# Kernel optimization log

Hardware: AMD Instinct MI355X
Metric: run time of the kernel (lower is better)

## Reference

```python
import jax, jax.numpy as jnp
import numpy as np

B, N, V, H = 8, 2048, 256, 1024
EPS = 1e-5
NEG = -1e9


def _layernorm(x, g, b):
    m = jnp.mean(x, axis=-1, keepdims=True)
    v = jnp.mean((x - m) ** 2, axis=-1, keepdims=True)
    return (x - m) / jnp.sqrt(v + EPS) * g + b


def setup_inputs() -> dict:
    key = jax.random.key(0)
    ks = jax.random.split(key, 10)
    tril = jnp.tril(jnp.ones((N, N), jnp.float32))
    return {
        "h": jax.random.normal(ks[0], (B, N, V), jnp.float32),
        "mask_one": tril,                      # keep causal entries
        "mask_zero": NEG * (1.0 - tril),       # -inf-ish above diagonal
        "ln_attn_g": jnp.ones((V,), jnp.float32),
        "ln_attn_b": jnp.zeros((V,), jnp.float32),
        "ln_mlp_g": jnp.ones((V,), jnp.float32),
        "ln_mlp_b": jnp.zeros((V,), jnp.float32),
        "wv": jax.random.normal(ks[1], (V,), jnp.float32),
        "wv_bos": jax.random.normal(ks[2], (V,), jnp.float32),
        "wo_w": jax.random.normal(ks[3], (V, V), jnp.float32) / np.sqrt(V),
        "qk_bos": jax.random.normal(ks[4], (V,), jnp.float32),
        "qk_previous": jax.random.normal(ks[5], (V,), jnp.float32),
        "qk_direction": jnp.ones((V,), jnp.float32),  # middel_layer=False, frozen
        "w1": jax.random.normal(ks[6], (H, V), jnp.float32) / np.sqrt(V),
        "w2": jax.random.normal(ks[7], (V, H), jnp.float32) / np.sqrt(H),
    }


def reference(h, mask_one, mask_zero, ln_attn_g, ln_attn_b, ln_mlp_g, ln_mlp_b,
              wv, wv_bos, wo_w, qk_bos, qk_previous, qk_direction, w1, w2):
    b, n, v = h.shape
    # mask blends LayerNorm only into row 0 (BOS position)
    attn_input = h.at[:, 0, :].set(_layernorm(h[:, 0, :], ln_attn_g, ln_attn_b))
    # value states: diag(wv) on positions 1.., wo(wv_bos) at position 0
    values = attn_input[:, 1:, :] * wv                      # [B, N-1, V]
    v_bos = wo_w @ wv_bos                                   # Linear(bias=False)
    values = jnp.concatenate(
        [jnp.broadcast_to(v_bos, (b, 1, v)), values], axis=1)  # [B, N, V]
    # sparse QK logits: column 0 term + sub-diagonal term, densified then masked
    col0 = (attn_input @ qk_bos) * (attn_input[:, 0, :] @ qk_direction)[:, None]  # [B, N]
    d = attn_input @ qk_previous                            # [B, N]
    qk = jnp.zeros((b, n, n), h.dtype).at[:, :, 0].add(col0)
    idx = jnp.arange(1, n)
    qk = qk.at[:, idx, idx - 1].add(d[:, 1:])               # row r, col r-1 = d[:, r]
    qk = qk * mask_one + mask_zero
    attn_out = jax.nn.softmax(qk, axis=-1) @ values         # [B, N, V]
    # FFN branch with its own BOS-only LayerNorm blend
    mlp_input = h.at[:, 0, :].set(_layernorm(h[:, 0, :], ln_mlp_g, ln_mlp_b))
    mlp_out = jax.nn.relu(mlp_input @ w1.T) @ w2.T          # [B, N, V]
    return attn_out + mlp_out
```

## Files before the change

kernel.cpp:

```cpp
#include <hip/hip_runtime.h>
#include <hip/hip_bf16.h>

#define BB 8
#define NN 2048
#define VV 256
#define HH 1024
#define CHK 64
#define RPC 32
constexpr float EPS = 1e-5f;

typedef __attribute__((ext_vector_type(4))) float floatx4;
typedef __attribute__((ext_vector_type(8))) short short8;

__device__ __forceinline__ void load_lds16(const void* g, void* l) {
    __builtin_amdgcn_global_load_lds((const __attribute__((address_space(1))) void*)g,
                                     (__attribute__((address_space(3))) void*)l, 16, 0, 0);
}

__global__ void prep_kernel(const float* __restrict__ h,
                            const float* __restrict__ g_attn, const float* __restrict__ b_attn,
                            const float* __restrict__ g_mlp,  const float* __restrict__ b_mlp,
                            const float* __restrict__ qk_dir,
                            const float* __restrict__ wo_w,  const float* __restrict__ wv_bos,
                            float* __restrict__ attn_row0, float* __restrict__ mlp_row0,
                            float* __restrict__ v_bos, float* __restrict__ sum0)
{
    int t = threadIdx.x;
    __shared__ float red[VV];
    if (blockIdx.x < BB) {
        int b = blockIdx.x;
        float x = h[(size_t)b * NN * VV + t];
        red[t] = x; __syncthreads();
        for (int s = 128; s > 0; s >>= 1) { if (t < s) red[t] += red[t + s]; __syncthreads(); }
        float m = red[0] * (1.0f / VV); __syncthreads();
        float xc = x - m;
        red[t] = xc * xc; __syncthreads();
        for (int s = 128; s > 0; s >>= 1) { if (t < s) red[t] += red[t + s]; __syncthreads(); }
        float var = red[0] * (1.0f / VV); __syncthreads();
        float inv = 1.0f / sqrtf(var + EPS);
        float an = xc * inv * g_attn[t] + b_attn[t];
        float mn = xc * inv * g_mlp[t] + b_mlp[t];
        attn_row0[b * VV + t] = an;
        mlp_row0[b * VV + t]  = mn;
        red[t] = an * qk_dir[t]; __syncthreads();
        for (int s = 128; s > 0; s >>= 1) { if (t < s) red[t] += red[t + s]; __syncthreads(); }
        if (t == 0) sum0[b] = red[0];
    } else {
        const float4* wp = reinterpret_cast<const float4*>(wo_w + (size_t)t * VV);
        const float4* vp = reinterpret_cast<const float4*>(wv_bos);
        float acc = 0.f;
        for (int j = 0; j < VV / 4; ++j) {
            float4 a = wp[j], b = vp[j];
            acc += a.x * b.x + a.y * b.y + a.z * b.z + a.w * b.w;
        }
        v_bos[t] = acc;
    }
}

__global__ void qkw_kernel(const float* __restrict__ h,
                           const float* __restrict__ qk_bos, const float* __restrict__ qk_prev,
                           const float* __restrict__ sum0,
                           float* __restrict__ w0, float* __restrict__ wprev, float* __restrict__ wz)
{
    int wave = threadIdx.x >> 6, lane = threadIdx.x & 63;
    int gid = blockIdx.x * 4 + wave;
    int b = gid >> 11, r = gid & (NN - 1);
    const float4* hp = reinterpret_cast<const float4*>(h + (size_t)gid * VV);
    float4 x = hp[lane];
    float4 qb = reinterpret_cast<const float4*>(qk_bos)[lane];
    float4 qp = reinterpret_cast<const float4*>(qk_prev)[lane];
    float s1 = x.x * qb.x + x.y * qb.y + x.z * qb.z + x.w * qb.w;
    float s2 = x.x * qp.x + x.y * qp.y + x.z * qp.z + x.w * qp.w;
    for (int off = 32; off > 0; off >>= 1) {
        s1 += __shfl_down(s1, off);
        s2 += __shfl_down(s2, off);
    }
    if (lane == 0) {
        float W0, WP, WZ;
        if (r == 0) { W0 = 1.f; WP = 0.f; WZ = 0.f; }
        else if (r == 1) {
            float a = s1 * sum0[b] + s2;
            float m = fmaxf(a, 0.f);
            float ea = expf(a - m), ez = expf(-m);
            float Z = ea + ez;
            W0 = ea / Z; WZ = ez / Z; WP = WZ;
        } else {
            float a = s1 * sum0[b];
            float dd = s2;
            float m = fmaxf(fmaxf(a, dd), 0.f);
            float ea = expf(a - m), ed = expf(dd - m), ez = expf(-m);
            float Z = ea + ed + (float)(r - 1) * ez;
            W0 = ea / Z; WP = ed / Z; WZ = ez / Z;
        }
        w0[gid] = W0; wprev[gid] = WP; wz[gid] = WZ;
    }
}

__global__ void chunksum_kernel(const float* __restrict__ h, const float* __restrict__ wv,
                                float* __restrict__ chunkSum)
{
    int b = blockIdx.x / CHK, c = blockIdx.x % CHK;
    int v = threadIdx.x;
    float wvv = wv[v];
    float s = 0.f;
    int r0 = c * RPC;
    for (int r = r0; r < r0 + RPC; ++r)
        if (r >= 1) s += h[((size_t)b * NN + r) * VV + v] * wvv;
    chunkSum[(b * CHK + c) * VV + v] = s;
}

__global__ void chunkscan_kernel(float* __restrict__ chunkSum)
{
    int b = blockIdx.x, v = threadIdx.x;
    float run = 0.f;
    for (int c = 0; c < CHK; ++c) {
        int idx = (b * CHK + c) * VV + v;
        float t = chunkSum[idx];
        chunkSum[idx] = run;
        run += t;
    }
}

__global__ void attn_kernel(const float* __restrict__ h, const float* __restrict__ wv,
                            const float* __restrict__ v_bos,
                            const float* __restrict__ w0, const float* __restrict__ wprev,
                            const float* __restrict__ wz, const float* __restrict__ chunkSum,
                            float* __restrict__ out)
{
    int b = blockIdx.x / CHK, c = blockIdx.x % CHK;
    int v = threadIdx.x;
    float wvv = wv[v], vb = v_bos[v];
    float S = chunkSum[(b * CHK + c) * VV + v];
    int r0 = c * RPC;
    float prev = (r0 == 0) ? 0.f : h[((size_t)b * NN + r0 - 1) * VV + v] * wvv;
    for (int r = r0; r < r0 + RPC; ++r) {
        size_t idx = ((size_t)b * NN + r) * VV + v;
        float o;
        if (r == 0) {
            o = vb;
            prev = 0.f;
        } else {
            float val = h[idx] * wvv;
            S += val;
            int wi = b * NN + r;
            o = w0[wi] * vb + (wprev[wi] - wz[wi]) * prev + wz[wi] * S;
            prev = val;
        }
        out[idx] = o;
    }
}

__global__ void cvt_x_kernel(const float* __restrict__ h, const float* __restrict__ mlp_row0,
                             __hip_bfloat16* __restrict__ Xb)
{
    int i = blockIdx.x * blockDim.x + threadIdx.x;
    int e = i * 4;
    int v = e & (VV - 1);
    int row = e >> 8;
    int r = row & (NN - 1), b = row >> 11;
    const float* src = (r == 0) ? (mlp_row0 + b * VV + v) : (h + (size_t)row * VV + v);
    float4 x = *reinterpret_cast<const float4*>(src);
    Xb[e + 0] = __float2bfloat16(x.x);
    Xb[e + 1] = __float2bfloat16(x.y);
    Xb[e + 2] = __float2bfloat16(x.z);
    Xb[e + 3] = __float2bfloat16(x.w);
}

__global__ void cvt_w_kernel(const float* __restrict__ w1, const float* __restrict__ w2,
                             __hip_bfloat16* __restrict__ w1b, __hip_bfloat16* __restrict__ w2b)
{
    int i = (blockIdx.x * blockDim.x + threadIdx.x) * 4;
    const float* src;
    __hip_bfloat16* dst;
    if (i < HH * VV) { src = w1 + i; dst = w1b + i; }
    else             { src = w2 + (i - HH * VV); dst = w2b + (i - HH * VV); }
    float4 x = *reinterpret_cast<const float4*>(src);
    dst[0] = __float2bfloat16(x.x);
    dst[1] = __float2bfloat16(x.y);
    dst[2] = __float2bfloat16(x.z);
    dst[3] = __float2bfloat16(x.w);
}

template<int BM, int BN, int K, int OUTN, bool FUSE_RELU_BF16>
__global__ __launch_bounds__(256) void mfma_gemm(const short* __restrict__ Ag,
                                                 const short* __restrict__ Bg,
                                                 __hip_bfloat16* __restrict__ Obf,
                                                 float* __restrict__ Ofp)
{
    constexpr int TM = BM / 2, TN = BN / 2;
    constexpr int MI = TM / 16, NJ = TN / 16;
    __shared__ __align__(16) short sA[BM * 32];
    __shared__ __align__(16) short sB[BN * 32];
    int wave = threadIdx.x >> 6, lane = threadIdx.x & 63;
    int wm = wave >> 1, wn = wave & 1;
    int m0 = blockIdx.x * BM, n0 = blockIdx.y * BN;

    int lrow = lane >> 2;
    int lp   = lane & 3;
    int ra   = lane & 15;
    int q    = lane >> 4;

    floatx4 acc[MI][NJ];
#pragma unroll
    for (int i = 0; i < MI; ++i)
#pragma unroll
        for (int j = 0; j < NJ; ++j) acc[i][j] = floatx4{0, 0, 0, 0};

    for (int k0 = 0; k0 < K; k0 += 32) {
#pragma unroll
        for (int i = 0; i < BM / 64; ++i) {
            int g = i * 4 + wave;
            int row = g * 16 + lrow;
            int s = lp ^ ((row >> 1) & 3);
            load_lds16(Ag + (size_t)(m0 + row) * K + k0 + s * 8, sA + g * 512);
        }
#pragma unroll
        for (int i = 0; i < BN / 64; ++i) {
            int g = i * 4 + wave;
            int row = g * 16 + lrow;
            int s = lp ^ ((row >> 1) & 3);
            load_lds16(Bg + (size_t)(n0 + row) * K + k0 + s * 8, sB + g * 512);
        }
        __syncthreads();

        short8 af[MI], bfr[NJ];
#pragma unroll
        for (int i = 0; i < MI; ++i) {
            int m = wm * TM + i * 16 + ra;
            int slot = q ^ ((m >> 1) & 3);
            af[i] = *reinterpret_cast<const short8*>(sA + m * 32 + slot * 8);
        }
#pragma unroll
        for (int j = 0; j < NJ; ++j) {
            int n = wn * TN + j * 16 + ra;
            int slot = q ^ ((n >> 1) & 3);
            bfr[j] = *reinterpret_cast<const short8*>(sB + n * 32 + slot * 8);
        }
#pragma unroll
        for (int i = 0; i < MI; ++i)
#pragma unroll
            for (int j = 0; j < NJ; ++j)
                acc[i][j] = __builtin_amdgcn_mfma_f32_16x16x32_bf16(af[i], bfr[j], acc[i][j], 0, 0, 0);
        __syncthreads();
    }

    int rq = q * 4;
#pragma unroll
    for (int i = 0; i < MI; ++i) {
        int rbase = m0 + wm * TM + i * 16 + rq;
#pragma unroll
        for (int j = 0; j < NJ; ++j) {
            int col = n0 + wn * TN + j * 16 + ra;
#pragma unroll
            for (int reg = 0; reg < 4; ++reg) {
                size_t idx = (size_t)(rbase + reg) * OUTN + col;
                if (FUSE_RELU_BF16)
                    Obf[idx] = __float2bfloat16(fmaxf(acc[i][j][reg], 0.f));
                else
                    Ofp[idx] += acc[i][j][reg];
            }
        }
    }
}

extern "C" void kernel_launch(void* const* d_in, const int* in_sizes, int n_in,
                              void* d_out, int out_size, void* d_ws, size_t ws_size,
                              hipStream_t stream)
{
    const float* h        = (const float*)d_in[0];
    const float* ln_attn_g = (const float*)d_in[3];
    const float* ln_attn_b = (const float*)d_in[4];
    const float* ln_mlp_g  = (const float*)d_in[5];
    const float* ln_mlp_b  = (const float*)d_in[6];
    const float* wv        = (const float*)d_in[7];
    const float* wv_bos    = (const float*)d_in[8];
    const float* wo_w      = (const float*)d_in[9];
    const float* qk_bos    = (const float*)d_in[10];
    const float* qk_prev   = (const float*)d_in[11];
    const float* qk_dir    = (const float*)d_in[12];
    const float* w1        = (const float*)d_in[13];
    const float* w2        = (const float*)d_in[14];
    float* out = (float*)d_out;

    float* attn_row0 = (float*)d_ws;
    float* mlp_row0  = attn_row0 + BB * VV;
    float* v_bos     = mlp_row0 + BB * VV;
    float* sum0      = v_bos + VV;
    float* w0        = sum0 + 8;
    float* wprev     = w0 + BB * NN;
    float* wzz       = wprev + BB * NN;
    float* chunkSum  = wzz + BB * NN;
    __hip_bfloat16* Xb  = (__hip_bfloat16*)(chunkSum + BB * CHK * VV);
    __hip_bfloat16* w1b = Xb + (size_t)BB * NN * VV;
    __hip_bfloat16* w2b = w1b + HH * VV;
    __hip_bfloat16* Yb  = w2b + VV * HH;

    prep_kernel<<<BB + 1, 256, 0, stream>>>(h, ln_attn_g, ln_attn_b, ln_mlp_g, ln_mlp_b,
                                            qk_dir, wo_w, wv_bos,
                                            attn_row0, mlp_row0, v_bos, sum0);
    cvt_x_kernel<<<(BB * NN * VV / 4) / 256, 256, 0, stream>>>(h, mlp_row0, Xb);
    cvt_w_kernel<<<(2 * HH * VV / 4) / 256, 256, 0, stream>>>(w1, w2, w1b, w2b);
    qkw_kernel<<<BB * NN / 4, 256, 0, stream>>>(h, qk_bos, qk_prev, sum0, w0, wprev, wzz);
    chunksum_kernel<<<BB * CHK, 256, 0, stream>>>(h, wv, chunkSum);
    chunkscan_kernel<<<BB, 256, 0, stream>>>(chunkSum);
    attn_kernel<<<BB * CHK, 256, 0, stream>>>(h, wv, v_bos, w0, wprev, wzz, chunkSum, out);

    mfma_gemm<128, 128, VV, HH, true>
        <<<dim3(BB * NN / 128, HH / 128), 256, 0, stream>>>(
            (const short*)Xb, (const short*)w1b, Yb, nullptr);
    mfma_gemm<128, 64, HH, VV, false>
        <<<dim3(BB * NN / 128, VV / 64), 256, 0, stream>>>(
            (const short*)Yb, (const short*)w2b, nullptr, out);
}
```

Measured before the change: 187.7 us.

## Fuse MLP GEMMs into one kernel and merge activation conversion with qk/scan prep

```diff
diff --git a/kernel.cpp b/kernel.cpp
--- a/kernel.cpp
+++ b/kernel.cpp
@@ -57,56 +57,73 @@
     }
 }
 
-__global__ void qkw_kernel(const float* __restrict__ h,
-                           const float* __restrict__ qk_bos, const float* __restrict__ qk_prev,
-                           const float* __restrict__ sum0,
-                           float* __restrict__ w0, float* __restrict__ wprev, float* __restrict__ wz)
-{
+__global__ __launch_bounds__(256) void scan_qkw_cvt_kernel(
+    const float* __restrict__ h, const float* __restrict__ mlp_row0,
+    const float* __restrict__ wv,
+    const float* __restrict__ qk_bos, const float* __restrict__ qk_prev,
+    const float* __restrict__ sum0,
+    short* __restrict__ Xb,
+    float* __restrict__ w0, float* __restrict__ wprev, float* __restrict__ wz,
+    float* __restrict__ chunkSum)
+{
+    __shared__ float lds[4][VV];
     int wave = threadIdx.x >> 6, lane = threadIdx.x & 63;
-    int gid = blockIdx.x * 4 + wave;
-    int b = gid >> 11, r = gid & (NN - 1);
-    const float4* hp = reinterpret_cast<const float4*>(h + (size_t)gid * VV);
-    float4 x = hp[lane];
-    float4 qb = reinterpret_cast<const float4*>(qk_bos)[lane];
-    float4 qp = reinterpret_cast<const float4*>(qk_prev)[lane];
-    float s1 = x.x * qb.x + x.y * qb.y + x.z * qb.z + x.w * qb.w;
-    float s2 = x.x * qp.x + x.y * qp.y + x.z * qp.z + x.w * qp.w;
-    for (int off = 32; off > 0; off >>= 1) {
-        s1 += __shfl_down(s1, off);
-        s2 += __shfl_down(s2, off);
-    }
-    if (lane == 0) {
-        float W0, WP, WZ;
-        if (r == 0) { W0 = 1.f; WP = 0.f; WZ = 0.f; }
-        else if (r == 1) {
-            float a = s1 * sum0[b] + s2;
-            float m = fmaxf(a, 0.f);
-            float ea = expf(a - m), ez = expf(-m);
-            float Z = ea + ez;
-            W0 = ea / Z; WZ = ez / Z; WP = WZ;
-        } else {
-            float a = s1 * sum0[b];
-            float dd = s2;
-            float m = fmaxf(fmaxf(a, dd), 0.f);
-            float ea = expf(a - m), ed = expf(dd - m), ez = expf(-m);
-            float Z = ea + ed + (float)(r - 1) * ez;
-            W0 = ea / Z; WP = ed / Z; WZ = ez / Z;
-        }
-        w0[gid] = W0; wprev[gid] = WP; wz[gid] = WZ;
-    }
-}
-
-__global__ void chunksum_kernel(const float* __restrict__ h, const float* __restrict__ wv,
-                                float* __restrict__ chunkSum)
-{
     int b = blockIdx.x / CHK, c = blockIdx.x % CHK;
+    int r0 = c * RPC + wave * 8;
+    float4 wv4 = reinterpret_cast<const float4*>(wv)[lane];
+    float4 qb4 = reinterpret_cast<const float4*>(qk_bos)[lane];
+    float4 qp4 = reinterpret_cast<const float4*>(qk_prev)[lane];
+    float s0b = sum0[b];
+    float4 vsum = {0.f, 0.f, 0.f, 0.f};
+#pragma unroll
+    for (int rr = 0; rr < 8; ++rr) {
+        int r = r0 + rr;
+        size_t base = ((size_t)b * NN + r) * VV;
+        float4 x = *reinterpret_cast<const float4*>(h + base + lane * 4);
+        float4 xs = x;
+        if (r == 0) xs = *reinterpret_cast<const float4*>(mlp_row0 + b * VV + lane * 4);
+        __hip_bfloat16 c0 = __float2bfloat16(xs.x), c1 = __float2bfloat16(xs.y),
+                       c2 = __float2bfloat16(xs.z), c3 = __float2bfloat16(xs.w);
+        short4 pk;
+        pk.x = *reinterpret_cast<short*>(&c0);
+        pk.y = *reinterpret_cast<short*>(&c1);
+        pk.z = *reinterpret_cast<short*>(&c2);
+        pk.w = *reinterpret_cast<short*>(&c3);
+        *reinterpret_cast<short4*>(Xb + base + lane * 4) = pk;
+        if (r != 0) {
+            vsum.x += x.x * wv4.x; vsum.y += x.y * wv4.y;
+            vsum.z += x.z * wv4.z; vsum.w += x.w * wv4.w;
+        }
+        float s1 = x.x * qb4.x + x.y * qb4.y + x.z * qb4.z + x.w * qb4.w;
+        float s2 = x.x * qp4.x + x.y * qp4.y + x.z * qp4.z + x.w * qp4.w;
+        for (int off = 32; off > 0; off >>= 1) {
+            s1 += __shfl_down(s1, off);
+            s2 += __shfl_down(s2, off);
+        }
+        if (lane == 0) {
+            int gid = b * NN + r;
+            float W0, WP, WZ;
+            if (r == 0) { W0 = 1.f; WP = 0.f; WZ = 0.f; }
+            else if (r == 1) {
+                float a = s1 * s0b + s2;
+                float m = fmaxf(a, 0.f);
+                float ea = expf(a - m), ez = expf(-m);
+                float Z = ea + ez;
+                W0 = ea / Z; WZ = ez / Z; WP = WZ;
+            } else {
+                float a = s1 * s0b;
+                float m = fmaxf(fmaxf(a, s2), 0.f);
+                float ea = expf(a - m), ed = expf(s2 - m), ez = expf(-m);
+                float Z = ea + ed + (float)(r - 1) * ez;
+                W0 = ea / Z; WP = ed / Z; WZ = ez / Z;
+            }
+            w0[gid] = W0; wprev[gid] = WP; wz[gid] = WZ;
+        }
+    }
+    reinterpret_cast<float4*>(lds[wave])[lane] = vsum;
+    __syncthreads();
     int v = threadIdx.x;
-    float wvv = wv[v];
-    float s = 0.f;
-    int r0 = c * RPC;
-    for (int r = r0; r < r0 + RPC; ++r)
-        if (r >= 1) s += h[((size_t)b * NN + r) * VV + v] * wvv;
-    chunkSum[(b * CHK + c) * VV + v] = s;
+    chunkSum[((size_t)b * CHK + c) * VV + v] = lds[0][v] + lds[1][v] + lds[2][v] + lds[3][v];
 }
 
 __global__ void chunkscan_kernel(float* __restrict__ chunkSum)
@@ -150,22 +167,6 @@
     }
 }
 
-__global__ void cvt_x_kernel(const float* __restrict__ h, const float* __restrict__ mlp_row0,
-                             __hip_bfloat16* __restrict__ Xb)
-{
-    int i = blockIdx.x * blockDim.x + threadIdx.x;
-    int e = i * 4;
-    int v = e & (VV - 1);
-    int row = e >> 8;
-    int r = row & (NN - 1), b = row >> 11;
-    const float* src = (r == 0) ? (mlp_row0 + b * VV + v) : (h + (size_t)row * VV + v);
-    float4 x = *reinterpret_cast<const float4*>(src);
-    Xb[e + 0] = __float2bfloat16(x.x);
-    Xb[e + 1] = __float2bfloat16(x.y);
-    Xb[e + 2] = __float2bfloat16(x.z);
-    Xb[e + 3] = __float2bfloat16(x.w);
-}
-
 __global__ void cvt_w_kernel(const float* __restrict__ w1, const float* __restrict__ w2,
                              __hip_bfloat16* __restrict__ w1b, __hip_bfloat16* __restrict__ w2b)
 {
@@ -181,83 +182,118 @@
     dst[3] = __float2bfloat16(x.w);
 }
 
-template<int BM, int BN, int K, int OUTN, bool FUSE_RELU_BF16>
-__global__ __launch_bounds__(256) void mfma_gemm(const short* __restrict__ Ag,
-                                                 const short* __restrict__ Bg,
-                                                 __hip_bfloat16* __restrict__ Obf,
-                                                 float* __restrict__ Ofp)
-{
-    constexpr int TM = BM / 2, TN = BN / 2;
-    constexpr int MI = TM / 16, NJ = TN / 16;
-    __shared__ __align__(16) short sA[BM * 32];
-    __shared__ __align__(16) short sB[BN * 32];
+__global__ __launch_bounds__(512) void mlp_fused(const short* __restrict__ Xb,
+                                                 const short* __restrict__ w1b,
+                                                 const short* __restrict__ w2b,
+                                                 float* __restrict__ out)
+{
+    __shared__ __align__(16) short sX[64 * 256];
+    __shared__ __align__(16) short sW1[64 * 256];
+    __shared__ __align__(16) short sW2[256 * 64];
+    __shared__ __align__(16) short sY[64 * 64];
     int wave = threadIdx.x >> 6, lane = threadIdx.x & 63;
-    int wm = wave >> 1, wn = wave & 1;
-    int m0 = blockIdx.x * BM, n0 = blockIdx.y * BN;
-
-    int lrow = lane >> 2;
-    int lp   = lane & 3;
-    int ra   = lane & 15;
-    int q    = lane >> 4;
-
-    floatx4 acc[MI][NJ];
-#pragma unroll
-    for (int i = 0; i < MI; ++i)
-#pragma unroll
-        for (int j = 0; j < NJ; ++j) acc[i][j] = floatx4{0, 0, 0, 0};
-
-    for (int k0 = 0; k0 < K; k0 += 32) {
-#pragma unroll
-        for (int i = 0; i < BM / 64; ++i) {
-            int g = i * 4 + wave;
-            int row = g * 16 + lrow;
-            int s = lp ^ ((row >> 1) & 3);
-            load_lds16(Ag + (size_t)(m0 + row) * K + k0 + s * 8, sA + g * 512);
-        }
-#pragma unroll
-        for (int i = 0; i < BN / 64; ++i) {
-            int g = i * 4 + wave;
-            int row = g * 16 + lrow;
-            int s = lp ^ ((row >> 1) & 3);
-            load_lds16(Bg + (size_t)(n0 + row) * K + k0 + s * 8, sB + g * 512);
-        }
+    int wm = wave >> 2, wn = wave & 3;
+    int m0 = blockIdx.x * 64;
+    int ra = lane & 15, q = lane >> 4;
+
+    floatx4 oacc[2][4];
+#pragma unroll
+    for (int i = 0; i < 2; ++i)
+#pragma unroll
+        for (int j = 0; j < 4; ++j) oacc[i][j] = floatx4{0.f, 0.f, 0.f, 0.f};
+
+    {
+        int rp = lane >> 5, segp = lane & 31;
+#pragma unroll
+        for (int i = 0; i < 4; ++i) {
+            int L = wave * 4 + i;
+            int row = L * 2 + rp;
+            int g = segp ^ (row & 7);
+            load_lds16(Xb + (size_t)(m0 + row) * 256 + g * 8, sX + L * 512);
+        }
+    }
+
+    for (int hc = 0; hc < 16; ++hc) {
         __syncthreads();
-
-        short8 af[MI], bfr[NJ];
-#pragma unroll
-        for (int i = 0; i < MI; ++i) {
-            int m = wm * TM + i * 16 + ra;
-            int slot = q ^ ((m >> 1) & 3);
-            af[i] = *reinterpret_cast<const short8*>(sA + m * 32 + slot * 8);
-        }
-#pragma unroll
-        for (int j = 0; j < NJ; ++j) {
-            int n = wn * TN + j * 16 + ra;
-            int slot = q ^ ((n >> 1) & 3);
-            bfr[j] = *reinterpret_cast<const short8*>(sB + n * 32 + slot * 8);
-        }
-#pragma unroll
-        for (int i = 0; i < MI; ++i)
-#pragma unroll
-            for (int j = 0; j < NJ; ++j)
-                acc[i][j] = __builtin_amdgcn_mfma_f32_16x16x32_bf16(af[i], bfr[j], acc[i][j], 0, 0, 0);
+        {
+            int rp = lane >> 5, segp = lane & 31;
+#pragma unroll
+            for (int i = 0; i < 4; ++i) {
+                int L = wave * 4 + i;
+                int row = L * 2 + rp;
+                int g = segp ^ (row & 7);
+                load_lds16(w1b + (size_t)(hc * 64 + row) * 256 + g * 8, sW1 + L * 512);
+            }
+            int rp2 = lane >> 3, segp2 = lane & 7;
+#pragma unroll
+            for (int i = 0; i < 4; ++i) {
+                int L = wave * 4 + i;
+                int row = L * 8 + rp2;
+                int g = segp2 ^ (row & 7);
+                load_lds16(w2b + (size_t)row * 1024 + hc * 64 + g * 8, sW2 + L * 512);
+            }
+        }
         __syncthreads();
-    }
-
-    int rq = q * 4;
-#pragma unroll
-    for (int i = 0; i < MI; ++i) {
-        int rbase = m0 + wm * TM + i * 16 + rq;
-#pragma unroll
-        for (int j = 0; j < NJ; ++j) {
-            int col = n0 + wn * TN + j * 16 + ra;
+
+        floatx4 yacc[2];
+        yacc[0] = floatx4{0.f, 0.f, 0.f, 0.f};
+        yacc[1] = floatx4{0.f, 0.f, 0.f, 0.f};
+#pragma unroll
+        for (int kk = 0; kk < 8; ++kk) {
+            int g = kk * 4 + q;
+            int n = wn * 16 + ra;
+            short8 bfr = *reinterpret_cast<const short8*>(sW1 + n * 256 + ((g ^ (n & 7)) * 8));
+#pragma unroll
+            for (int i = 0; i < 2; ++i) {
+                int m = wm * 32 + i * 16 + ra;
+                short8 a = *reinterpret_cast<const short8*>(sX + m * 256 + ((g ^ (m & 7)) * 8));
+                yacc[i] = __builtin_amdgcn_mfma_f32_16x16x32_bf16(a, bfr, yacc[i], 0, 0, 0);
+            }
+        }
+
+#pragma unroll
+        for (int i = 0; i < 2; ++i) {
 #pragma unroll
             for (int reg = 0; reg < 4; ++reg) {
-                size_t idx = (size_t)(rbase + reg) * OUTN + col;
-                if (FUSE_RELU_BF16)
-                    Obf[idx] = __float2bfloat16(fmaxf(acc[i][j][reg], 0.f));
-                else
-                    Ofp[idx] += acc[i][j][reg];
+                int me = wm * 32 + i * 16 + q * 4 + reg;
+                int ke = wn * 16 + ra;
+                float v = fmaxf(yacc[i][reg], 0.f);
+                __hip_bfloat16 hb = __float2bfloat16(v);
+                sY[me * 64 + (((ke >> 3) ^ (me & 7)) * 8) + (ke & 7)] =
+                    *reinterpret_cast<short*>(&hb);
+            }
+        }
+        __syncthreads();
+
+#pragma unroll
+        for (int kk2 = 0; kk2 < 2; ++kk2) {
+            int g = kk2 * 4 + q;
+            short8 a2[2];
+#pragma unroll
+            for (int i = 0; i < 2; ++i) {
+                int m = wm * 32 + i * 16 + ra;
+                a2[i] = *reinterpret_cast<const short8*>(sY + m * 64 + ((g ^ (m & 7)) * 8));
+            }
+#pragma unroll
+            for (int j = 0; j < 4; ++j) {
+                int n = wn * 64 + j * 16 + ra;
+                short8 b2 = *reinterpret_cast<const short8*>(sW2 + n * 64 + ((g ^ (n & 7)) * 8));
+#pragma unroll
+                for (int i = 0; i < 2; ++i)
+                    oacc[i][j] = __builtin_amdgcn_mfma_f32_16x16x32_bf16(a2[i], b2, oacc[i][j], 0, 0, 0);
+            }
+        }
+    }
+
+#pragma unroll
+    for (int i = 0; i < 2; ++i) {
+#pragma unroll
+        for (int j = 0; j < 4; ++j) {
+#pragma unroll
+            for (int reg = 0; reg < 4; ++reg) {
+                int row = m0 + wm * 32 + i * 16 + q * 4 + reg;
+                int col = wn * 64 + j * 16 + ra;
+                out[(size_t)row * VV + col] += oacc[i][j][reg];
             }
         }
     }
@@ -290,25 +326,17 @@
     float* wprev     = w0 + BB * NN;
     float* wzz       = wprev + BB * NN;
     float* chunkSum  = wzz + BB * NN;
-    __hip_bfloat16* Xb  = (__hip_bfloat16*)(chunkSum + BB * CHK * VV);
-    __hip_bfloat16* w1b = Xb + (size_t)BB * NN * VV;
-    __hip_bfloat16* w2b = w1b + HH * VV;
-    __hip_bfloat16* Yb  = w2b + VV * HH;
+    short* Xb            = (short*)(chunkSum + BB * CHK * VV);
+    __hip_bfloat16* w1b  = (__hip_bfloat16*)(Xb + (size_t)BB * NN * VV);
+    __hip_bfloat16* w2b  = w1b + HH * VV;
 
     prep_kernel<<<BB + 1, 256, 0, stream>>>(h, ln_attn_g, ln_attn_b, ln_mlp_g, ln_mlp_b,
                                             qk_dir, wo_w, wv_bos,
                                             attn_row0, mlp_row0, v_bos, sum0);
-    cvt_x_kernel<<<(BB * NN * VV / 4) / 256, 256, 0, stream>>>(h, mlp_row0, Xb);
     cvt_w_kernel<<<(2 * HH * VV / 4) / 256, 256, 0, stream>>>(w1, w2, w1b, w2b);
-    qkw_kernel<<<BB * NN / 4, 256, 0, stream>>>(h, qk_bos, qk_prev, sum0, w0, wprev, wzz);
-    chunksum_kernel<<<BB * CHK, 256, 0, stream>>>(h, wv, chunkSum);
+    scan_qkw_cvt_kernel<<<BB * CHK, 256, 0, stream>>>(h, mlp_row0, wv, qk_bos, qk_prev,
+                                                      sum0, Xb, w0, wprev, wzz, chunkSum);
     chunkscan_kernel<<<BB, 256, 0, stream>>>(chunkSum);
     attn_kernel<<<BB * CHK, 256, 0, stream>>>(h, wv, v_bos, w0, wprev, wzz, chunkSum, out);
-
-    mfma_gemm<128, 128, VV, HH, true>
-        <<<dim3(BB * NN / 128, HH / 128), 256, 0, stream>>>(
-            (const short*)Xb, (const short*)w1b, Yb, nullptr);
-    mfma_gemm<128, 64, HH, VV, false>
-        <<<dim3(BB * NN / 128, VV / 64), 256, 0, stream>>>(
-            (const short*)Yb, (const short*)w2b, nullptr, out);
-}
+    mlp_fused<<<256, 512, 0, stream>>>(Xb, (const short*)w1b, (const short*)w2b, out);
+}
```

After: 182.3 us. 2.9% less time.
